# Optimization experiments

Hardware: AMD Instinct MI355X
Metric: run time of the kernel (lower is better)

## Reference

```python
import jax, jax.numpy as jnp
import numpy as np

N_NODES = 50000
N_EDGES = 800000
NODE_FEAT = 176
EDGE_FEAT = 4
HIDDEN = 64
LAYERS = 4
LN_EPS = 1e-5


def setup_inputs() -> dict:
    key = jax.random.key(0)
    ks = jax.random.split(key, 20)
    H, H2, Hh = HIDDEN, HIDDEN * 2, HIDDEN // 2
    inp = {
        "x": jax.random.normal(ks[0], (N_NODES, NODE_FEAT), jnp.float32),
        "edge_index": jax.random.randint(ks[1], (2, N_EDGES), 0, N_NODES, jnp.int64),
        "edge_attr": jax.random.normal(ks[2], (N_EDGES, EDGE_FEAT), jnp.float32),
        # input projection
        "in_w": jax.random.normal(ks[3], (NODE_FEAT, H), jnp.float32) * 0.05,
        "in_b": jnp.zeros((H,), jnp.float32),
        # per-layer GINEConv params (stacked over LAYERS)
        "edge_w": jax.random.normal(ks[4], (LAYERS, EDGE_FEAT, H), jnp.float32) * 0.1,
        "edge_b": jnp.zeros((LAYERS, H), jnp.float32),
        "mlp_w1": jax.random.normal(ks[5], (LAYERS, H, H2), jnp.float32) * 0.05,
        "mlp_b1": jnp.zeros((LAYERS, H2), jnp.float32),
        "mlp_w2": jax.random.normal(ks[6], (LAYERS, H2, H), jnp.float32) * 0.05,
        "mlp_b2": jnp.zeros((LAYERS, H), jnp.float32),
        "ln_g": jnp.ones((LAYERS, H), jnp.float32),
        "ln_b": jnp.zeros((LAYERS, H), jnp.float32),
        "reg_w1": jax.random.normal(ks[7], (H, Hh), jnp.float32) * 0.1,
        "reg_b1": jnp.zeros((Hh,), jnp.float32),
        "reg_w2": jax.random.normal(ks[8], (Hh, 1), jnp.float32) * 0.1,
        "reg_b2": jnp.zeros((1,), jnp.float32),
    }
    return inp


def _layernorm(z, g, b):
    mu = jnp.mean(z, axis=-1, keepdims=True)
    var = jnp.mean((z - mu) ** 2, axis=-1, keepdims=True)
    return g * (z - mu) * jax.lax.rsqrt(var + LN_EPS) + b


def reference(x, edge_index, edge_attr, in_w, in_b, edge_w, edge_b,
              mlp_w1, mlp_b1, mlp_w2, mlp_b2, ln_g, ln_b,
              reg_w1, reg_b1, reg_w2, reg_b2):
    src, dst = edge_index[0], edge_index[1]
    h = x @ in_w + in_b  # [N, H]
    for l in range(LAYERS):
        e = edge_attr @ edge_w[l] + edge_b[l]              # [E, H] edge projection
        msg = jax.nn.relu(h[src] + e)                      # gather + relu
        aggr = jax.ops.segment_sum(msg, dst, num_segments=h.shape[0])  # scatter-add
        z = h + aggr                                       # (1+eps)*x_i + aggr, eps=0
        z = jax.nn.relu(z @ mlp_w1[l] + mlp_b1[l]) @ mlp_w2[l] + mlp_b2[l]
        h = jax.nn.relu(_layernorm(z, ln_g[l], ln_b[l]))
    g = jnp.sum(h, axis=0)                                 # global_add_pool, single graph
    out = jax.nn.relu(g @ reg_w1 + reg_b1) @ reg_w2 + reg_b2
    return out.squeeze()
```

## Files before the change

kernel.cpp:

```cpp
#include <hip/hip_runtime.h>

#define N_NODES 50000
#define N_EDGES 800000
#define NODE_FEAT 176
#define HIDDEN 64
#define LN_EPS 1e-5f
#define SCAN_NB 49

typedef short bf16x8 __attribute__((ext_vector_type(8)));
typedef float f32x4 __attribute__((ext_vector_type(4)));
typedef long long ll2 __attribute__((ext_vector_type(2)));

__device__ __forceinline__ unsigned short f2bf(float f) {
    unsigned int u = __float_as_uint(f);
    u += 0x7FFFu + ((u >> 16) & 1u);
    return (unsigned short)(u >> 16);
}
__device__ __forceinline__ int pack2(float lo, float hi) {
    return (int)(((unsigned)f2bf(hi) << 16) | (unsigned)f2bf(lo));
}
__device__ __forceinline__ float bf2f(unsigned short s) {
    return __uint_as_float(((unsigned int)s) << 16);
}

#if __has_builtin(__builtin_amdgcn_cvt_pk_fp8_f32) && __has_builtin(__builtin_amdgcn_cvt_f32_fp8)
#define HW_FP8 1
#endif

__device__ __forceinline__ unsigned char f2fp8(float f) {
#ifdef HW_FP8
    return (unsigned char)(__builtin_amdgcn_cvt_pk_fp8_f32(f, f, 0, false) & 0xff);
#else
    unsigned u = __float_as_uint(f);
    unsigned s = (u >> 24) & 0x80u;
    float a = fabsf(f);
    if (a >= 448.f) return (unsigned char)(s | 0x7E);
    if (a < 0.0078125f) {
        int m = (int)fmaf(a, 512.0f, 0.5f);
        return (unsigned char)(s | (m > 7 ? 7 : m));
    }
    unsigned au = u & 0x7fffffffu;
    au += 0x7ffffu + ((au >> 20) & 1u);
    int e8 = (int)(au >> 23) - 120;
    if (e8 <= 0) {
        int m = (int)fmaf(__uint_as_float(au), 512.0f, 0.5f);
        return (unsigned char)(s | (m > 7 ? 7 : m));
    }
    if (e8 > 15) return (unsigned char)(s | 0x7E);
    return (unsigned char)(s | (e8 << 3) | ((au >> 20) & 7));
#endif
}
__device__ __forceinline__ float fp82f(int b) {
#ifdef HW_FP8
    return __builtin_amdgcn_cvt_f32_fp8(b & 0xff, 0);
#else
    int s = (b >> 7) & 1, e = (b >> 3) & 15, m = b & 7;
    float v = e ? __uint_as_float(((unsigned)(e + 120) << 23) | ((unsigned)m << 20))
                : (float)m * 0.001953125f;
    return s ? -v : v;
#endif
}

__device__ __forceinline__ float wave_sum64(float v) {
#pragma unroll
    for (int o = 32; o > 0; o >>= 1) v += __shfl_xor(v, o);
    return v;
}
__device__ __forceinline__ float sum16(float v) {
#pragma unroll
    for (int o = 8; o > 0; o >>= 1) v += __shfl_xor(v, o);
    return v;
}

__global__ __launch_bounds__(256) void k_wprep(const float* __restrict__ in_w,
                                               const float* __restrict__ w1,
                                               const float* __restrict__ w2,
                                               unsigned short* __restrict__ fin,
                                               unsigned short* __restrict__ f1,
                                               unsigned short* __restrict__ f2,
                                               int* __restrict__ cnt) {
    int t = blockIdx.x * 256 + threadIdx.x;
    if (t < N_NODES) {
        int4 z = {0, 0, 0, 0};
        int4* p = (int4*)(cnt + ((size_t)t << 4));
        p[0] = z; p[1] = z; p[2] = z; p[3] = z;
    }
    if (t < 12288) {
        int e = t;
        int r = e & 7, lane = (e >> 3) & 63, j = (e >> 9) & 3, s = e >> 11;
        int k = s * 32 + ((lane >> 4) << 3) + r;
        int n = (j << 4) + (lane & 15);
        fin[e] = (k < NODE_FEAT) ? f2bf(in_w[k * 64 + n]) : (unsigned short)0;
    } else if (t < 12288 + 32768) {
        int e = t - 12288;
        int L = e >> 13, e2 = e & 8191;
        int r = e2 & 7, lane = (e2 >> 3) & 63, j = (e2 >> 9) & 7, s = (e2 >> 12) & 1;
        int k = s * 32 + ((lane >> 4) << 3) + r;
        int n = (j << 4) + (lane & 15);
        f1[e] = f2bf(w1[L * 8192 + k * 128 + n]);
    } else if (t < 12288 + 32768 + 32768) {
        int e = t - 45056;
        int L = e >> 13, e2 = e & 8191;
        int r = e2 & 7, lane = (e2 >> 3) & 63, j = (e2 >> 9) & 3, s = (e2 >> 11) & 3;
        int k = s * 32 + ((lane >> 4) << 3) + r;
        int n = (j << 4) + (lane & 15);
        f2[e] = f2bf(w2[L * 8192 + k * 64 + n]);
    }
}

__global__ __launch_bounds__(256) void k_inproj_mfma(const float* __restrict__ x,
                                                     const unsigned short* __restrict__ wfrag,
                                                     const float* __restrict__ in_b,
                                                     unsigned short* __restrict__ hb,
                                                     unsigned char* __restrict__ hf8) {
    __shared__ unsigned short lw[12288];
    const int tid = threadIdx.x;
    {
        const bf16x8* src = (const bf16x8*)wfrag;
        bf16x8* dst = (bf16x8*)lw;
        for (int i = tid; i < 1536; i += 256) dst[i] = src[i];
    }
    __syncthreads();
    const int wv = tid >> 6, lane = tid & 63;
    const int lrow = lane & 15, lgrp = lane >> 4;
    float ib[4];
#pragma unroll
    for (int j = 0; j < 4; ++j) ib[j] = in_b[16 * j + lrow];
    const int nwaves = gridDim.x * 4;
    for (int tile = blockIdx.x * 4 + wv; tile < 3125; tile += nwaves) {
        const int m0 = tile * 16;
        f32x4 acc[4];
#pragma unroll
        for (int j = 0; j < 4; ++j) acc[j] = (f32x4){ib[j], ib[j], ib[j], ib[j]};
#pragma unroll
        for (int s = 0; s < 6; ++s) {
            const int kbase = s * 32 + lgrp * 8;
            bf16x8 a;
            if (kbase < NODE_FEAT) {
                const float* p = x + (size_t)(m0 + lrow) * NODE_FEAT + kbase;
                float4 fa = *(const float4*)p;
                float4 fb = *(const float4*)(p + 4);
                a[0] = (short)f2bf(fa.x); a[1] = (short)f2bf(fa.y);
                a[2] = (short)f2bf(fa.z); a[3] = (short)f2bf(fa.w);
                a[4] = (short)f2bf(fb.x); a[5] = (short)f2bf(fb.y);
                a[6] = (short)f2bf(fb.z); a[7] = (short)f2bf(fb.w);
            } else {
                a = (bf16x8){0, 0, 0, 0, 0, 0, 0, 0};
            }
#pragma unroll
            for (int j = 0; j < 4; ++j) {
                bf16x8 b = *(const bf16x8*)&lw[((s * 4 + j) * 64 + lane) * 8];
                acc[j] = __builtin_amdgcn_mfma_f32_16x16x32_bf16(a, b, acc[j], 0, 0, 0);
            }
        }
#pragma unroll
        for (int j = 0; j < 4; ++j) {
            const int col = 16 * j + lrow;
#pragma unroll
            for (int r = 0; r < 4; ++r) {
                const int node = m0 + lgrp * 4 + r;
                float v = acc[j][r];
                __builtin_nontemporal_store(f2bf(v), &hb[(size_t)node * 64 + col]);
                hf8[(size_t)node * 64 + col] = f2fp8(v);
            }
        }
    }
}

__global__ __launch_bounds__(256) void k_hist(const int* __restrict__ ei,
                                              int* __restrict__ cnt,
                                              int* __restrict__ erank) {
    int e = blockIdx.x * 256 + threadIdx.x;
    if (e < N_EDGES) erank[e] = atomicAdd(&cnt[ei[N_EDGES + e] << 4], 1);
}

__global__ __launch_bounds__(256) void k_scan_part(const int* __restrict__ cnt,
                                                   int* __restrict__ blksum) {
    const int b = blockIdx.x, t = threadIdx.x;
    const int base = b * 1024 + t * 4;
    int s = 0;
#pragma unroll
    for (int i = 0; i < 4; ++i) {
        int idx = base + i;
        if (idx < N_NODES) s += cnt[idx << 4];
    }
#pragma unroll
    for (int o = 32; o > 0; o >>= 1) s += __shfl_xor(s, o);
    __shared__ int wt[4];
    if ((t & 63) == 0) wt[t >> 6] = s;
    __syncthreads();
    if (t == 0) blksum[b] = wt[0] + wt[1] + wt[2] + wt[3];
}

__global__ __launch_bounds__(256) void k_scan_add(const int* __restrict__ cnt,
                                                  const int* __restrict__ blksum,
                                                  int* __restrict__ row_ptr) {
    const int b = blockIdx.x, t = threadIdx.x;
    __shared__ int boff_s;
    if (t < 64) {
        int v = (t < SCAN_NB) ? blksum[t] : 0;
        int incl = v;
#pragma unroll
        for (int o = 1; o < 64; o <<= 1) {
            int u = __shfl_up(incl, o);
            if (t >= o) incl += u;
        }
        if (t == b) boff_s = incl - v;
        if (b == 0 && t == 63) row_ptr[N_NODES] = incl;
    }
    __syncthreads();
    const int base = b * 1024 + t * 4;
    int c[4];
    int tsum = 0;
#pragma unroll
    for (int i = 0; i < 4; ++i) {
        int idx = base + i;
        c[i] = (idx < N_NODES) ? cnt[idx << 4] : 0;
        tsum += c[i];
    }
    int incl = tsum;
#pragma unroll
    for (int o = 1; o < 64; o <<= 1) {
        int u = __shfl_up(incl, o);
        if ((t & 63) >= o) incl += u;
    }
    __shared__ int wt[4];
    const int wv = t >> 6;
    if ((t & 63) == 63) wt[wv] = incl;
    __syncthreads();
    int run = boff_s + (incl - tsum);
    for (int w = 0; w < wv; ++w) run += wt[w];
#pragma unroll
    for (int i = 0; i < 4; ++i) {
        int idx = base + i;
        if (idx < N_NODES) row_ptr[idx] = run;
        run += c[i];
    }
}

__global__ __launch_bounds__(256) void k_scatter(const int* __restrict__ ei,
                                                 const float4* __restrict__ ea,
                                                 const int* __restrict__ row_ptr,
                                                 const int* __restrict__ erank,
                                                 int4* __restrict__ rec) {
    int e = blockIdx.x * 256 + threadIdx.x;
    if (e >= N_EDGES) return;
    int d = ei[N_EDGES + e];
    float4 a = ea[e];
    int4 r;
    r.x = pack2(a.x, a.y);
    r.y = pack2(a.z, a.w);
    r.z = ei[e];
    r.w = 0;
    rec[row_ptr[d] + erank[e]] = r;
}

__global__ __launch_bounds__(256) void k_aggr(const unsigned short* __restrict__ hb_in,
                                              const unsigned char* __restrict__ hf8_in,
                                              unsigned short* __restrict__ zb,
                                              const int* __restrict__ row_ptr,
                                              const int4* __restrict__ rec,
                                              const float* __restrict__ ew,
                                              const float* __restrict__ eb) {
    const int wv = threadIdx.x >> 6, lane = threadIdx.x & 63;
    const int node = blockIdx.x * 4 + wv;
    const float ew0 = ew[0 * 64 + lane], ew1 = ew[1 * 64 + lane];
    const float ew2 = ew[2 * 64 + lane], ew3 = ew[3 * 64 + lane];
    const float ebl = eb[lane];
    const int beg = __builtin_amdgcn_readfirstlane(row_ptr[node]);
    const int end = __builtin_amdgcn_readfirstlane(row_ptr[node + 1]);
    float acc = bf2f(__builtin_nontemporal_load(&hb_in[(size_t)node * 64 + lane]));
    int i = beg;
    for (; i + 8 <= end; i += 8) {
        int d0[8], d1[8], sx[8];
#pragma unroll
        for (int t = 0; t < 8; ++t) {
            ll2 r = __builtin_nontemporal_load((const ll2*)(rec + i + t));
            d0[t] = __builtin_amdgcn_readfirstlane((int)(r[0] & 0xffffffffLL));
            d1[t] = __builtin_amdgcn_readfirstlane((int)(r[0] >> 32));
            sx[t] = __builtin_amdgcn_readfirstlane((int)(r[1] & 0xffffffffLL));
        }
        float gg[8];
#pragma unroll
        for (int t = 0; t < 8; ++t)
            gg[t] = fp82f(hf8_in[((size_t)sx[t] << 6) + lane]);
#pragma unroll
        for (int t = 0; t < 8; ++t) {
            float a0 = __uint_as_float((unsigned)d0[t] << 16);
            float a1 = __uint_as_float((unsigned)d0[t] & 0xffff0000u);
            float a2 = __uint_as_float((unsigned)d1[t] << 16);
            float a3 = __uint_as_float((unsigned)d1[t] & 0xffff0000u);
            float v = fmaf(a0, ew0, fmaf(a1, ew1, fmaf(a2, ew2, fmaf(a3, ew3, ebl))));
            acc += fmaxf(v + gg[t], 0.0f);
        }
    }
    if (i < end) {
        const int n = end - i;
        int d0[8], d1[8], sx[8];
#pragma unroll
        for (int t = 0; t < 8; ++t) {
            int idx = i + ((t < n) ? t : (n - 1));
            ll2 r = __builtin_nontemporal_load((const ll2*)(rec + idx));
            d0[t] = __builtin_amdgcn_readfirstlane((int)(r[0] & 0xffffffffLL));
            d1[t] = __builtin_amdgcn_readfirstlane((int)(r[0] >> 32));
            sx[t] = __builtin_amdgcn_readfirstlane((int)(r[1] & 0xffffffffLL));
        }
        float gg[8];
#pragma unroll
        for (int t = 0; t < 8; ++t)
            gg[t] = fp82f(hf8_in[((size_t)sx[t] << 6) + lane]);
#pragma unroll
        for (int t = 0; t < 8; ++t) {
            float m = (t < n) ? 1.0f : 0.0f;
            float a0 = __uint_as_float((unsigned)d0[t] << 16);
            float a1 = __uint_as_float((unsigned)d0[t] & 0xffff0000u);
            float a2 = __uint_as_float((unsigned)d1[t] << 16);
            float a3 = __uint_as_float((unsigned)d1[t] & 0xffff0000u);
            float v = fmaf(a0, ew0, fmaf(a1, ew1, fmaf(a2, ew2, fmaf(a3, ew3, ebl))));
            acc += m * fmaxf(v + gg[t], 0.0f);
        }
    }
    __builtin_nontemporal_store(f2bf(acc), &zb[(size_t)node * 64 + lane]);
}

__global__ __launch_bounds__(256) void k_mlp_mfma(const unsigned short* __restrict__ zb,
                                                  unsigned short* __restrict__ hb_out,
                                                  unsigned char* __restrict__ hf8_out,
                                                  const unsigned short* __restrict__ f1,
                                                  const unsigned short* __restrict__ f2,
                                                  const float* __restrict__ b1,
                                                  const float* __restrict__ b2,
                                                  const float* __restrict__ lng,
                                                  const float* __restrict__ lnb) {
    __shared__ unsigned short w1f[8192];
    __shared__ unsigned short w2f[8192];
    __shared__ unsigned short z1s[4][2048];
    const int tid = threadIdx.x;
    {
        const bf16x8* s1 = (const bf16x8*)f1;
        const bf16x8* s2 = (const bf16x8*)f2;
        bf16x8* d1 = (bf16x8*)w1f;
        bf16x8* d2 = (bf16x8*)w2f;
        for (int i = tid; i < 1024; i += 256) { d1[i] = s1[i]; d2[i] = s2[i]; }
    }
    __syncthreads();
    const int wv = tid >> 6, lane = tid & 63;
    const int lrow = lane & 15, lgrp = lane >> 4;
    unsigned short* zs = z1s[wv];
    float bb1[8], bb2[4], g4[4], be4[4];
#pragma unroll
    for (int j = 0; j < 8; ++j) bb1[j] = b1[16 * j + lrow];
#pragma unroll
    for (int j = 0; j < 4; ++j) {
        bb2[j] = b2[16 * j + lrow];
        g4[j] = lng[16 * j + lrow];
        be4[j] = lnb[16 * j + lrow];
    }
    const int nwaves = gridDim.x * 4;
    for (int tile = blockIdx.x * 4 + wv; tile < 3125; tile += nwaves) {
        const int m0 = tile * 16;
        f32x4 acc1[8];
#pragma unroll
    for (int j = 0; j < 8; ++j) acc1[j] = (f32x4){bb1[j], bb1[j], bb1[j], bb1[j]};
#pragma unroll
        for (int s = 0; s < 2; ++s) {
            const int kbase = s * 32 + lgrp * 8;
            bf16x8 a = *(const bf16x8*)&zb[(size_t)(m0 + lrow) * 64 + kbase];
#pragma unroll
            for (int j = 0; j < 8; ++j) {
                bf16x8 b = *(const bf16x8*)&w1f[((s * 8 + j) * 64 + lane) * 8];
                acc1[j] = __builtin_amdgcn_mfma_f32_16x16x32_bf16(a, b, acc1[j], 0, 0, 0);
            }
        }
#pragma unroll
        for (int j = 0; j < 8; ++j) {
            const int col = 16 * j + lrow;
#pragma unroll
            for (int r = 0; r < 4; ++r) {
                const int row = lgrp * 4 + r;
                const int idx = (row * 128 + col) ^ ((row & 7) << 3);
                zs[idx] = f2bf(fmaxf(acc1[j][r], 0.0f));
            }
        }
        f32x4 acc2[4];
#pragma unroll
        for (int j = 0; j < 4; ++j) acc2[j] = (f32x4){bb2[j], bb2[j], bb2[j], bb2[j]};
#pragma unroll
        for (int s = 0; s < 4; ++s) {
            const int kbase = s * 32 + lgrp * 8;
            const int idx = (lrow * 128 + kbase) ^ ((lrow & 7) << 3);
            bf16x8 a = *(const bf16x8*)&zs[idx];
#pragma unroll
            for (int j = 0; j < 4; ++j) {
                bf16x8 b = *(const bf16x8*)&w2f[((s * 4 + j) * 64 + lane) * 8];
                acc2[j] = __builtin_amdgcn_mfma_f32_16x16x32_bf16(a, b, acc2[j], 0, 0, 0);
            }
        }
#pragma unroll
        for (int r = 0; r < 4; ++r) {
            float sum = acc2[0][r] + acc2[1][r] + acc2[2][r] + acc2[3][r];
            sum = sum16(sum);
            const float mu = sum * (1.0f / 64.0f);
            float sq = 0.0f;
#pragma unroll
            for (int j = 0; j < 4; ++j) {
                float d = acc2[j][r] - mu;
                sq = fmaf(d, d, sq);
            }
            sq = sum16(sq);
            const float rstd = rsqrtf(sq * (1.0f / 64.0f) + LN_EPS);
            const int node = m0 + lgrp * 4 + r;
#pragma unroll
            for (int j = 0; j < 4; ++j) {
                const int col = 16 * j + lrow;
                float d = acc2[j][r] - mu;
                float hn = fmaxf(fmaf(g4[j] * d, rstd, be4[j]), 0.0f);
                __builtin_nontemporal_store(f2bf(hn), &hb_out[(size_t)node * 64 + col]);
                hf8_out[(size_t)node * 64 + col] = f2fp8(hn);
            }
        }
    }
}

__global__ __launch_bounds__(256) void k_pool(const unsigned short* __restrict__ hb,
                                              float* __restrict__ gpart) {
    __shared__ float red[256];
    const int tid = threadIdx.x;
    const int lane = tid & 63;
    float part = 0.0f;
    for (int i = blockIdx.x * 4 + (tid >> 6); i < N_NODES; i += gridDim.x * 4)
        part += bf2f(hb[(size_t)i * 64 + lane]);
    red[tid] = part;
    __syncthreads();
    if (tid < 64) {
        gpart[blockIdx.x * 64 + tid] = red[tid] + red[tid + 64] + red[tid + 128] + red[tid + 192];
    }
}

__global__ __launch_bounds__(64) void k_reg(const float* __restrict__ gpart,
                                            const float* __restrict__ w1,
                                            const float* __restrict__ b1,
                                            const float* __restrict__ w2,
                                            const float* __restrict__ b2,
                                            float* __restrict__ out) {
    const int j = threadIdx.x;
    float gj = 0.0f;
    for (int b = 0; b < 256; ++b) gj += gpart[b * 64 + j];
    __shared__ float gs[64];
    gs[j] = gj;
    __syncthreads();
    const int jm = j & 31;
    float acc = b1[jm];
#pragma unroll 8
    for (int k = 0; k < 64; ++k) {
        float gk = gs[k];
        acc = fmaf(gk, w1[k * 32 + jm], acc);
    }
    float contrib = (j < 32) ? fmaxf(acc, 0.0f) * w2[jm] : 0.0f;
    float s = wave_sum64(contrib);
    if (j == 0) out[0] = s + b2[0];
}

extern "C" void kernel_launch(void* const* d_in, const int* in_sizes, int n_in,
                              void* d_out, int out_size, void* d_ws, size_t ws_size,
                              hipStream_t stream) {
    const float* x      = (const float*)d_in[0];
    const int*   ei     = (const int*)d_in[1];
    const float* ea     = (const float*)d_in[2];
    const float* in_w   = (const float*)d_in[3];
    const float* in_b   = (const float*)d_in[4];
    const float* edge_w = (const float*)d_in[5];
    const float* edge_b = (const float*)d_in[6];
    const float* mlp_w1 = (const float*)d_in[7];
    const float* mlp_b1 = (const float*)d_in[8];
    const float* mlp_w2 = (const float*)d_in[9];
    const float* mlp_b2 = (const float*)d_in[10];
    const float* ln_g   = (const float*)d_in[11];
    const float* ln_b   = (const float*)d_in[12];
    const float* reg_w1 = (const float*)d_in[13];
    const float* reg_b1 = (const float*)d_in[14];
    const float* reg_w2 = (const float*)d_in[15];
    const float* reg_b2 = (const float*)d_in[16];

    char* ws = (char*)d_ws;
    unsigned short* hb0     = (unsigned short*)ws; ws += (size_t)N_NODES * 64 * 2;
    unsigned short* hb1     = (unsigned short*)ws; ws += (size_t)N_NODES * 64 * 2;
    unsigned short* zb      = (unsigned short*)ws; ws += (size_t)N_NODES * 64 * 2;
    unsigned char*  hf8_0   = (unsigned char*)ws;  ws += (size_t)N_NODES * 64;
    unsigned char*  hf8_1   = (unsigned char*)ws;  ws += (size_t)N_NODES * 64;
    int4*           rec     = (int4*)ws;           ws += (size_t)N_EDGES * 16;
    unsigned short* fin     = (unsigned short*)ws; ws += 12288 * 2;
    unsigned short* f1      = (unsigned short*)ws; ws += 32768 * 2;
    unsigned short* f2      = (unsigned short*)ws; ws += 32768 * 2;
    int*            erank   = (int*)ws;            ws += (size_t)N_EDGES * 4;
    int*            row_ptr = (int*)ws;            ws += (size_t)(N_NODES + 1) * 4;
    int*            cnt     = (int*)ws;            ws += (size_t)N_NODES * 16 * 4;
    int*            blksum  = (int*)ws;            ws += SCAN_NB * 4;
    float*          gpart   = (float*)ws;          ws += 256 * 64 * 4;
    float*          outf    = (float*)d_out;

    const int eb_blocks = (N_EDGES + 255) / 256;

    k_wprep<<<304, 256, 0, stream>>>(in_w, mlp_w1, mlp_w2, fin, f1, f2, cnt);

    k_hist<<<eb_blocks, 256, 0, stream>>>(ei, cnt, erank);
    k_scan_part<<<SCAN_NB, 256, 0, stream>>>(cnt, blksum);
    k_scan_add<<<SCAN_NB, 256, 0, stream>>>(cnt, blksum, row_ptr);
    k_scatter<<<eb_blocks, 256, 0, stream>>>(ei, (const float4*)ea, row_ptr, erank, rec);

    k_inproj_mfma<<<512, 256, 0, stream>>>(x, fin, in_b, hb0, hf8_0);

    unsigned short* hbA = hb0;
    unsigned short* hbB = hb1;
    unsigned char*  hfA = hf8_0;
    unsigned char*  hfB = hf8_1;
    for (int l = 0; l < 4; ++l) {
        k_aggr<<<N_NODES / 4, 256, 0, stream>>>(hbA, hfA, zb, row_ptr, rec,
                                                edge_w + l * 4 * 64,
                                                edge_b + l * 64);
        k_mlp_mfma<<<768, 256, 0, stream>>>(zb, hbB, hfB,
                                            f1 + l * 8192, f2 + l * 8192,
                                            mlp_b1 + l * 128, mlp_b2 + l * 64,
                                            ln_g + l * 64, ln_b + l * 64);
        unsigned short* tb = hbA; hbA = hbB; hbB = tb;
        unsigned char*  tf = hfA; hfA = hfB; hfB = tf;
    }

    k_pool<<<256, 256, 0, stream>>>(hbA, gpart);
    k_reg<<<1, 64, 0, stream>>>(gpart, reg_w1, reg_b1, reg_w2, reg_b2, outf);
}
```

Measured before the change: 271.5 us.

## Use scalar record loads in aggregation, fuse regressor into pool, retune grids

The aggregation kernel now reads edge records and the fp8 feature base through wave-uniform pointers with readfirstlane. This lets the compiler issue scalar loads in place of per-lane nontemporal vector loads. The separate regressor kernel is folded into the pool kernel: a last-block ticket counter, reset in the weight-prep kernel, picks the block that runs it, which removes one launch. The histogram kernel now processes two edges per thread, and the MLP grid size changes from 768 to 782 blocks. Risks are the ticket/threadfence ordering and a barrier executed by only part of the last block.

```diff
diff --git a/kernel.cpp b/kernel.cpp
--- a/kernel.cpp
+++ b/kernel.cpp
@@ -9,7 +9,6 @@
 
 typedef short bf16x8 __attribute__((ext_vector_type(8)));
 typedef float f32x4 __attribute__((ext_vector_type(4)));
-typedef long long ll2 __attribute__((ext_vector_type(2)));
 
 __device__ __forceinline__ unsigned short f2bf(float f) {
     unsigned int u = __float_as_uint(f);
@@ -71,6 +70,14 @@
     for (int o = 8; o > 0; o >>= 1) v += __shfl_xor(v, o);
     return v;
 }
+__device__ __forceinline__ int rfl(int v) { return __builtin_amdgcn_readfirstlane(v); }
+template <typename T>
+__device__ __forceinline__ const T* uniform_ptr(const T* p) {
+    unsigned long long u = (unsigned long long)p;
+    unsigned lo = __builtin_amdgcn_readfirstlane((unsigned)u);
+    unsigned hi = __builtin_amdgcn_readfirstlane((unsigned)(u >> 32));
+    return (const T*)(((unsigned long long)hi << 32) | lo);
+}
 
 __global__ __launch_bounds__(256) void k_wprep(const float* __restrict__ in_w,
                                                const float* __restrict__ w1,
@@ -78,8 +85,10 @@
                                                unsigned short* __restrict__ fin,
                                                unsigned short* __restrict__ f1,
                                                unsigned short* __restrict__ f2,
-                                               int* __restrict__ cnt) {
+                                               int* __restrict__ cnt,
+                                               int* __restrict__ ticket) {
     int t = blockIdx.x * 256 + threadIdx.x;
+    if (t == 0) ticket[0] = 0;
     if (t < N_NODES) {
         int4 z = {0, 0, 0, 0};
         int4* p = (int4*)(cnt + ((size_t)t << 4));
@@ -170,8 +179,10 @@
 __global__ __launch_bounds__(256) void k_hist(const int* __restrict__ ei,
                                               int* __restrict__ cnt,
                                               int* __restrict__ erank) {
-    int e = blockIdx.x * 256 + threadIdx.x;
+    int e = blockIdx.x * 512 + threadIdx.x;
     if (e < N_EDGES) erank[e] = atomicAdd(&cnt[ei[N_EDGES + e] << 4], 1);
+    int e2 = e + 256;
+    if (e2 < N_EDGES) erank[e2] = atomicAdd(&cnt[ei[N_EDGES + e2] << 4], 1);
 }
 
 __global__ __launch_bounds__(256) void k_scan_part(const int* __restrict__ cnt,
@@ -267,23 +278,25 @@
     const float ew0 = ew[0 * 64 + lane], ew1 = ew[1 * 64 + lane];
     const float ew2 = ew[2 * 64 + lane], ew3 = ew[3 * 64 + lane];
     const float ebl = eb[lane];
-    const int beg = __builtin_amdgcn_readfirstlane(row_ptr[node]);
-    const int end = __builtin_amdgcn_readfirstlane(row_ptr[node + 1]);
+    const int beg = rfl(row_ptr[node]);
+    const int end = rfl(row_ptr[node + 1]);
+    const int4* recu = uniform_ptr(rec);
+    const unsigned char* hfu = uniform_ptr(hf8_in);
     float acc = bf2f(__builtin_nontemporal_load(&hb_in[(size_t)node * 64 + lane]));
     int i = beg;
     for (; i + 8 <= end; i += 8) {
         int d0[8], d1[8], sx[8];
 #pragma unroll
         for (int t = 0; t < 8; ++t) {
-            ll2 r = __builtin_nontemporal_load((const ll2*)(rec + i + t));
-            d0[t] = __builtin_amdgcn_readfirstlane((int)(r[0] & 0xffffffffLL));
-            d1[t] = __builtin_amdgcn_readfirstlane((int)(r[0] >> 32));
-            sx[t] = __builtin_amdgcn_readfirstlane((int)(r[1] & 0xffffffffLL));
+            int4 r = recu[i + t];
+            d0[t] = rfl(r.x);
+            d1[t] = rfl(r.y);
+            sx[t] = rfl(r.z);
         }
         float gg[8];
 #pragma unroll
         for (int t = 0; t < 8; ++t)
-            gg[t] = fp82f(hf8_in[((size_t)sx[t] << 6) + lane]);
+            gg[t] = fp82f(hfu[((size_t)(unsigned)sx[t] << 6) + lane]);
 #pragma unroll
         for (int t = 0; t < 8; ++t) {
             float a0 = __uint_as_float((unsigned)d0[t] << 16);
@@ -300,15 +313,15 @@
 #pragma unroll
         for (int t = 0; t < 8; ++t) {
             int idx = i + ((t < n) ? t : (n - 1));
-            ll2 r = __builtin_nontemporal_load((const ll2*)(rec + idx));
-            d0[t] = __builtin_amdgcn_readfirstlane((int)(r[0] & 0xffffffffLL));
-            d1[t] = __builtin_amdgcn_readfirstlane((int)(r[0] >> 32));
-            sx[t] = __builtin_amdgcn_readfirstlane((int)(r[1] & 0xffffffffLL));
+            int4 r = recu[idx];
+            d0[t] = rfl(r.x);
+            d1[t] = rfl(r.y);
+            sx[t] = rfl(r.z);
         }
         float gg[8];
 #pragma unroll
         for (int t = 0; t < 8; ++t)
-            gg[t] = fp82f(hf8_in[((size_t)sx[t] << 6) + lane]);
+            gg[t] = fp82f(hfu[((size_t)(unsigned)sx[t] << 6) + lane]);
 #pragma unroll
         for (int t = 0; t < 8; ++t) {
             float m = (t < n) ? 1.0f : 0.0f;
@@ -361,7 +374,7 @@
         const int m0 = tile * 16;
         f32x4 acc1[8];
 #pragma unroll
-    for (int j = 0; j < 8; ++j) acc1[j] = (f32x4){bb1[j], bb1[j], bb1[j], bb1[j]};
+        for (int j = 0; j < 8; ++j) acc1[j] = (f32x4){bb1[j], bb1[j], bb1[j], bb1[j]};
 #pragma unroll
         for (int s = 0; s < 2; ++s) {
             const int kbase = s * 32 + lgrp * 8;
@@ -423,7 +436,13 @@
 }
 
 __global__ __launch_bounds__(256) void k_pool(const unsigned short* __restrict__ hb,
-                                              float* __restrict__ gpart) {
+                                              float* __restrict__ gpart,
+                                              int* __restrict__ ticket,
+                                              const float* __restrict__ w1,
+                                              const float* __restrict__ b1,
+                                              const float* __restrict__ w2,
+                                              const float* __restrict__ b2,
+                                              float* __restrict__ out) {
     __shared__ float red[256];
     const int tid = threadIdx.x;
     const int lane = tid & 63;
@@ -435,30 +454,25 @@
     if (tid < 64) {
         gpart[blockIdx.x * 64 + tid] = red[tid] + red[tid + 64] + red[tid + 128] + red[tid + 192];
     }
-}
-
-__global__ __launch_bounds__(64) void k_reg(const float* __restrict__ gpart,
-                                            const float* __restrict__ w1,
-                                            const float* __restrict__ b1,
-                                            const float* __restrict__ w2,
-                                            const float* __restrict__ b2,
-                                            float* __restrict__ out) {
-    const int j = threadIdx.x;
-    float gj = 0.0f;
-    for (int b = 0; b < 256; ++b) gj += gpart[b * 64 + j];
-    __shared__ float gs[64];
-    gs[j] = gj;
-    __syncthreads();
-    const int jm = j & 31;
-    float acc = b1[jm];
+    __threadfence();
+    __shared__ int amLast;
+    if (tid == 0) amLast = (atomicAdd(ticket, 1) == 255);
+    __syncthreads();
+    if (amLast && tid < 64) {
+        __threadfence();
+        float gj = 0.0f;
+        for (int b = 0; b < 256; ++b) gj += gpart[b * 64 + tid];
+        __shared__ float gs[64];
+        gs[tid] = gj;
+        __syncthreads();
+        const int jm = tid & 31;
+        float acc = b1[jm];
 #pragma unroll 8
-    for (int k = 0; k < 64; ++k) {
-        float gk = gs[k];
-        acc = fmaf(gk, w1[k * 32 + jm], acc);
-    }
-    float contrib = (j < 32) ? fmaxf(acc, 0.0f) * w2[jm] : 0.0f;
-    float s = wave_sum64(contrib);
-    if (j == 0) out[0] = s + b2[0];
+        for (int k = 0; k < 64; ++k) acc = fmaf(gs[k], w1[k * 32 + jm], acc);
+        float contrib = (tid < 32) ? fmaxf(acc, 0.0f) * w2[jm] : 0.0f;
+        float s = wave_sum64(contrib);
+        if (tid == 0) out[0] = s + b2[0];
+    }
 }
 
 extern "C" void kernel_launch(void* const* d_in, const int* in_sizes, int n_in,
@@ -496,14 +510,16 @@
     int*            row_ptr = (int*)ws;            ws += (size_t)(N_NODES + 1) * 4;
     int*            cnt     = (int*)ws;            ws += (size_t)N_NODES * 16 * 4;
     int*            blksum  = (int*)ws;            ws += SCAN_NB * 4;
+    int*            ticket  = (int*)ws;            ws += 64;
     float*          gpart   = (float*)ws;          ws += 256 * 64 * 4;
     float*          outf    = (float*)d_out;
 
     const int eb_blocks = (N_EDGES + 255) / 256;
-
-    k_wprep<<<304, 256, 0, stream>>>(in_w, mlp_w1, mlp_w2, fin, f1, f2, cnt);
-
-    k_hist<<<eb_blocks, 256, 0, stream>>>(ei, cnt, erank);
+    const int h2_blocks = (N_EDGES + 511) / 512;
+
+    k_wprep<<<304, 256, 0, stream>>>(in_w, mlp_w1, mlp_w2, fin, f1, f2, cnt, ticket);
+
+    k_hist<<<h2_blocks, 256, 0, stream>>>(ei, cnt, erank);
     k_scan_part<<<SCAN_NB, 256, 0, stream>>>(cnt, blksum);
     k_scan_add<<<SCAN_NB, 256, 0, stream>>>(cnt, blksum, row_ptr);
     k_scatter<<<eb_blocks, 256, 0, stream>>>(ei, (const float4*)ea, row_ptr, erank, rec);
@@ -518,7 +534,7 @@
         k_aggr<<<N_NODES / 4, 256, 0, stream>>>(hbA, hfA, zb, row_ptr, rec,
                                                 edge_w + l * 4 * 64,
                                                 edge_b + l * 64);
-        k_mlp_mfma<<<768, 256, 0, stream>>>(zb, hbB, hfB,
+        k_mlp_mfma<<<782, 256, 0, stream>>>(zb, hbB, hfB,
                                             f1 + l * 8192, f2 + l * 8192,
                                             mlp_b1 + l * 128, mlp_b2 + l * 64,
                                             ln_g + l * 64, ln_b + l * 64);
@@ -526,6 +542,6 @@
         unsigned char*  tf = hfA; hfA = hfB; hfB = tf;
     }
 
-    k_pool<<<256, 256, 0, stream>>>(hbA, gpart);
-    k_reg<<<1, 64, 0, stream>>>(gpart, reg_w1, reg_b1, reg_w2, reg_b2, outf);
-}
+    k_pool<<<256, 256, 0, stream>>>(hbA, gpart, ticket,
+                                    reg_w1, reg_b1, reg_w2, reg_b2, outf);
+}
```

Result: slower. 299.5 us (+10.3%).
